# Kernel tuning notes

Hardware: AMD Instinct MI355X
Metric: run time of the kernel (lower is better)

Reference implementation:

```python
import jax, jax.numpy as jnp
import numpy as np

N = 50000
E = 800000
IN_C, HID_C, OUT_C = 128, 256, 2


def sage_conv(x, src, dst, W_l, b_l, W_r, num_nodes):
    # PyG SAGEConv with mean aggregation:
    #   out = lin_l(mean_{j in N(i)} x_j) + lin_r(x_i)
    msg = x[src]                                            # [E, d] gather
    agg = jax.ops.segment_sum(msg, dst, num_segments=num_nodes)   # [N, d]
    cnt = jax.ops.segment_sum(jnp.ones((msg.shape[0],), x.dtype), dst,
                              num_segments=num_nodes)        # [N]
    agg = agg / jnp.maximum(cnt, 1.0)[:, None]               # mean (deg>=1)
    return agg @ W_l.T + b_l + x @ W_r.T


def setup_inputs() -> dict:
    key = jax.random.key(0)
    ks = jax.random.split(key, 8)
    x = jax.random.normal(ks[0], (N, IN_C), dtype=jnp.float32)
    edge_index = jax.random.randint(ks[1], (2, E), 0, N, dtype=jnp.int32)
    # glorot-ish scaled params
    s1 = 1.0 / np.sqrt(IN_C)
    s2 = 1.0 / np.sqrt(HID_C)
    W1l = jax.random.normal(ks[2], (HID_C, IN_C), dtype=jnp.float32) * s1
    W1r = jax.random.normal(ks[3], (HID_C, IN_C), dtype=jnp.float32) * s1
    b1 = jnp.zeros((HID_C,), dtype=jnp.float32)
    W2l = jax.random.normal(ks[4], (OUT_C, HID_C), dtype=jnp.float32) * s2
    W2r = jax.random.normal(ks[5], (OUT_C, HID_C), dtype=jnp.float32) * s2
    b2 = jnp.zeros((OUT_C,), dtype=jnp.float32)
    return {"x": x, "edge_index": edge_index,
            "W1l": W1l, "b1": b1, "W1r": W1r,
            "W2l": W2l, "b2": b2, "W2r": W2r}


def reference(x, edge_index, W1l, b1, W1r, W2l, b2, W2r):
    src, dst = edge_index[0], edge_index[1]
    h = sage_conv(x, src, dst, W1l, b1, W1r, N)
    h = jax.nn.relu(h)
    out = sage_conv(h, src, dst, W2l, b2, W2r, N)
    return out
```

## Files before the change

kernel.cpp:

```cpp
#include <hip/hip_runtime.h>
#include <hip/hip_bf16.h>


#define IN_C 128
#define HID_C 256
#define BKT_SHIFT 7
#define BKT_W 128
#define CAP 3072

typedef __attribute__((ext_vector_type(8))) short short8;
typedef __attribute__((ext_vector_type(4))) float f32x4;

static __device__ __forceinline__ unsigned short f2b(float f) {
    __hip_bfloat16 h = __float2bfloat16(f);
    return *(unsigned short*)&h;
}
static __device__ __forceinline__ float b2f(unsigned short u) {
    unsigned v = ((unsigned)u) << 16;
    return *(float*)&v;
}

__global__ __launch_bounds__(512) void scatter_conv(
    const float* __restrict__ x, unsigned int* __restrict__ Abf,
    const float* __restrict__ w1l, const float* __restrict__ w1r,
    unsigned short* __restrict__ Bg,
    const int* __restrict__ ei, int* __restrict__ bcnt,
    unsigned int* __restrict__ binned,
    int npairs , int xblk, int E_) {
    __shared__ int hist[512];
    __shared__ int lbase[512];
    const int tid = threadIdx.x;
    if (blockIdx.x < xblk) {
        int t = blockIdx.x * 512 + tid;
        if (t >= npairs) return;
        float2 v = *(const float2*)&x[(size_t)t * 2];
        unsigned int o = ((unsigned)f2b(v.y) << 16) | f2b(v.x);
        int node = t >> 6, g = t & 63;
        Abf[(size_t)node * 128 + 64 + g] = o;
    } else if (blockIdx.x < xblk + 128) {
        int idx = (blockIdx.x - xblk) * 512 + tid;
        int o = idx >> 8, k = idx & 255;
        float f = (k < IN_C) ? w1l[o * IN_C + k] : w1r[o * IN_C + (k - IN_C)];
        Bg[idx] = f2b(f);
    } else {
        const int e0 = (blockIdx.x - xblk - 128) * 2048;
        hist[tid] = 0;
        __syncthreads();
        int dreg[4];
#pragma unroll
        for (int j = 0; j < 4; ++j) {
            int e = e0 + j * 512 + tid;
            dreg[j] = (e < E_) ? ei[E_ + e] : -1;
            if (dreg[j] >= 0) atomicAdd(&hist[dreg[j] >> BKT_SHIFT], 1);
        }
        __syncthreads();
        {
            int c = hist[tid];
            lbase[tid] = c ? tid * CAP + atomicAdd(&bcnt[tid], c) : 0;
            hist[tid] = 0;
        }
        __syncthreads();
#pragma unroll
        for (int j = 0; j < 4; ++j) {
            int e = e0 + j * 512 + tid;
            if (dreg[j] >= 0) {
                int d = dreg[j];
                int b = d >> BKT_SHIFT;
                int pos = lbase[b] + atomicAdd(&hist[b], 1);
                if (pos < b * CAP + CAP)
                    binned[pos] = ((unsigned)ei[e] << BKT_SHIFT) |
                                  (unsigned)(d & (BKT_W - 1));
            }
        }
    }
}


__global__ __launch_bounds__(1024) void sort_gather(
    unsigned int* __restrict__ binned, const int* __restrict__ bcnt,
    const uint4* __restrict__ abf4c, uint4* __restrict__ Abf4,
    int* __restrict__ deg, int* __restrict__ boffs, int n) {
    __shared__ unsigned int ebuf[CAP];
    __shared__ unsigned short sbuf[CAP];
    __shared__ int hist[BKT_W];
    __shared__ int offs[BKT_W];
    __shared__ int cur[BKT_W];
    const int tid = threadIdx.x;
    const int lane = tid & 63;
    const int bkt = blockIdx.x;
    const int gbase = bkt * CAP;
    int cnt = bcnt[bkt];
    if (cnt > CAP) cnt = CAP;

    if (tid < BKT_W) hist[tid] = 0;
    for (int i = tid; i < cnt; i += 1024) ebuf[i] = binned[gbase + i];
    __syncthreads();
    for (int i = tid; i < cnt; i += 1024)
        atomicAdd(&hist[ebuf[i] & (BKT_W - 1)], 1);
    __syncthreads();
    if (tid < 64) {
        int h0 = hist[lane * 2], h1 = hist[lane * 2 + 1];
        int s = h0 + h1;
        int incl = s;
#pragma unroll
        for (int off = 1; off < 64; off <<= 1) {
            int t = __shfl_up(incl, off);
            if (lane >= off) incl += t;
        }
        int excl = incl - s;
        offs[lane * 2] = excl;          cur[lane * 2] = excl;
        offs[lane * 2 + 1] = excl + h0; cur[lane * 2 + 1] = excl + h0;
    }
    __syncthreads();
    for (int i = tid; i < cnt; i += 1024) {
        unsigned int pk = ebuf[i];
        int pos = atomicAdd(&cur[pk & (BKT_W - 1)], 1);
        sbuf[pos] = (unsigned short)(pk >> BKT_SHIFT);
    }
    if (tid < BKT_W) {
        int node = bkt * BKT_W + tid;
        if (node < n) { deg[node] = hist[tid]; boffs[node] = offs[tid]; }
    }
    __syncthreads();

    {
        unsigned short* sout = (unsigned short*)(binned + gbase);
        for (int i = tid; i < cnt; i += 1024) sout[i] = sbuf[i];
    }

    const int wv = tid >> 6;
    const int ep = lane >> 4;
    const int pos = lane & 15;
    for (int ld = wv * 8; ld < wv * 8 + 8; ++ld) {
        int node = bkt * BKT_W + ld;
        if (node >= n) break;
        int beg = offs[ld], end = offs[ld] + hist[ld];
        float s[8] = {0.f, 0.f, 0.f, 0.f, 0.f, 0.f, 0.f, 0.f};
        for (int e = beg; e < end; e += 8) {
#pragma unroll
            for (int g = 0; g < 2; ++g) {
                int eg = e + g * 4 + ep;
                if (eg < end) {
                    int src = sbuf[eg];
                    uint4 u = abf4c[(size_t)src * 32 + 16 + pos];
                    s[0] += b2f(u.x & 0xffff); s[1] += b2f(u.x >> 16);
                    s[2] += b2f(u.y & 0xffff); s[3] += b2f(u.y >> 16);
                    s[4] += b2f(u.z & 0xffff); s[5] += b2f(u.z >> 16);
                    s[6] += b2f(u.w & 0xffff); s[7] += b2f(u.w >> 16);
                }
            }
        }
#pragma unroll
        for (int i = 0; i < 8; ++i) {
            s[i] += __shfl_xor(s[i], 16);
            s[i] += __shfl_xor(s[i], 32);
        }
        if (ep == 0) {
            float inv = 1.0f / (float)max(end - beg, 1);
            uint4 o;
            o.x = ((unsigned)f2b(s[1] * inv) << 16) | f2b(s[0] * inv);
            o.y = ((unsigned)f2b(s[3] * inv) << 16) | f2b(s[2] * inv);
            o.z = ((unsigned)f2b(s[5] * inv) << 16) | f2b(s[4] * inv);
            o.w = ((unsigned)f2b(s[7] * inv) << 16) | f2b(s[6] * inv);
            Abf4[(size_t)node * 32 + pos] = o;
        }
    }
}


#define LSTR 72

__global__ __launch_bounds__(256) void gemm1_fused(
    const unsigned short* __restrict__ Abf, const unsigned short* __restrict__ Bg,
    const float* __restrict__ b1, const float* __restrict__ w2l,
    const float* __restrict__ w2r, float* __restrict__ p2g,
    float* __restrict__ rsg, int nn) {
    __shared__ short As[128 * LSTR];
    __shared__ short Bs[128 * LSTR];

    const int tid = threadIdx.x;
    const int lane = tid & 63;
    const int wid = tid >> 6;
    const int wm = wid >> 1, wn = wid & 1;
    const int row0 = blockIdx.x * 128;
    const int col0 = blockIdx.y * 128;

    const int srow = tid >> 1;
    const int skc = (tid & 1) * 32;
    int arow = row0 + srow;
    if (arow >= nn) arow = nn - 1;
    const size_t agoff = (size_t)arow * 256 + skc;
    const size_t bgoff = (size_t)(col0 + srow) * 256 + skc;

    f32x4 acc[4][4];
#pragma unroll
    for (int i = 0; i < 4; ++i)
#pragma unroll
        for (int j = 0; j < 4; ++j) acc[i][j] = (f32x4){0.f, 0.f, 0.f, 0.f};

    const int quad = lane >> 4;
    const int l16 = lane & 15;

    for (int k0 = 0; k0 < 256; k0 += 64) {
        const uint4* ga = (const uint4*)(Abf + agoff + k0);
        const uint4* gb = (const uint4*)(Bg + bgoff + k0);
        uint4 va0 = ga[0], va1 = ga[1], va2 = ga[2], va3 = ga[3];
        uint4 vb0 = gb[0], vb1 = gb[1], vb2 = gb[2], vb3 = gb[3];

        __syncthreads();
        uint4* la = (uint4*)&As[srow * LSTR + skc];
        uint4* lb = (uint4*)&Bs[srow * LSTR + skc];
        la[0] = va0; la[1] = va1; la[2] = va2; la[3] = va3;
        lb[0] = vb0; lb[1] = vb1; lb[2] = vb2; lb[3] = vb3;
        __syncthreads();

#pragma unroll
        for (int kb = 0; kb < 2; ++kb) {
            short8 af[4], bf[4];
#pragma unroll
            for (int mt = 0; mt < 4; ++mt)
                af[mt] = *(const short8*)&As[(wm * 64 + mt * 16 + l16) * LSTR + kb * 32 + quad * 8];
#pragma unroll
            for (int nt = 0; nt < 4; ++nt)
                bf[nt] = *(const short8*)&Bs[(wn * 64 + nt * 16 + l16) * LSTR + kb * 32 + quad * 8];
#pragma unroll
            for (int mt = 0; mt < 4; ++mt)
#pragma unroll
                for (int nt = 0; nt < 4; ++nt)
                    acc[mt][nt] = __builtin_amdgcn_mfma_f32_16x16x32_bf16(
                        af[mt], bf[nt], acc[mt][nt], 0, 0, 0);
        }
    }

    const int cbase = col0 + wn * 64 + l16;
#pragma unroll
    for (int half = 0; half < 2; ++half) {
        const float* wA = half ? w2r : w2l;
        float* og = half ? rsg : p2g;
        f32x4 part[2][4];
#pragma unroll
        for (int c = 0; c < 2; ++c)
#pragma unroll
            for (int mt = 0; mt < 4; ++mt) part[c][mt] = (f32x4){0.f, 0.f, 0.f, 0.f};
#pragma unroll
        for (int nt = 0; nt < 4; ++nt) {
            const int col = cbase + nt * 16;
            const float bias = b1[col];
            const float w0 = wA[col];
            const float w1 = wA[HID_C + col];
#pragma unroll
            for (int mt = 0; mt < 4; ++mt)
#pragma unroll
                for (int r = 0; r < 4; ++r) {
                    float hv = fmaxf(acc[mt][nt][r] + bias, 0.0f);
                    part[0][mt][r] += hv * w0;
                    part[1][mt][r] += hv * w1;
                }
        }
#pragma unroll
        for (int c = 0; c < 2; ++c)
#pragma unroll
            for (int mt = 0; mt < 4; ++mt)
#pragma unroll
                for (int r = 0; r < 4; ++r)
#pragma unroll
                    for (int m = 1; m < 16; m <<= 1)
                        part[c][mt][r] += __shfl_xor(part[c][mt][r], m);
        if (l16 < 8) {
            const int ch2 = l16 & 1;
            const int mts = l16 >> 1;
#pragma unroll
            for (int r = 0; r < 4; ++r) {
                int row = row0 + wm * 64 + quad * 4 + mts * 16 + r;
                if (row < nn)
                    atomicAdd(&og[row * 2 + ch2], part[ch2][mts][r]);
            }
        }
    }
}


__global__ __launch_bounds__(256) void fin_bucket(
    const unsigned int* __restrict__ binned, const int* __restrict__ boffs,
    const int* __restrict__ deg,
    const float2* __restrict__ p2, const float2* __restrict__ rs,
    const float* __restrict__ b2, float* __restrict__ out, int n) {
    __shared__ float ps0[BKT_W];
    __shared__ float ps1[BKT_W];
    const int tid = threadIdx.x;
    const int ln = tid & (BKT_W - 1);
    const int hp = tid >> 7;
    const int bkt = blockIdx.x;
    const int node = bkt * BKT_W + ln;
    const unsigned short* sp =
        (const unsigned short*)(binned + (size_t)bkt * CAP);
    float s0 = 0.f, s1 = 0.f;
    int dg = 0;
    if (node < n) {
        int beg = boffs[node];
        dg = deg[node];
        int end = beg + dg;
        for (int i = beg + hp; i < end; i += 2) {
            float2 v = p2[sp[i]];
            s0 += v.x; s1 += v.y;
        }
    }
    if (hp) { ps0[ln] = s0; ps1[ln] = s1; }
    __syncthreads();
    if (!hp && node < n) {
        s0 += ps0[ln]; s1 += ps1[ln];
        float inv = 1.0f / (float)max(dg, 1);
        float2 self = rs[node];
        out[node * 2 + 0] = s0 * inv + self.x + b2[0];
        out[node * 2 + 1] = s1 * inv + self.y + b2[1];
    }
}


extern "C" void kernel_launch(void* const* d_in, const int* in_sizes, int n_in,
                              void* d_out, int out_size, void* d_ws, size_t ws_size,
                              hipStream_t stream) {
    const float* x   = (const float*)d_in[0];
    const int*   ei  = (const int*)d_in[1];
    const float* W1l = (const float*)d_in[2];
    const float* b1  = (const float*)d_in[3];
    const float* W1r = (const float*)d_in[4];
    const float* W2l = (const float*)d_in[5];
    const float* b2  = (const float*)d_in[6];
    const float* W2r = (const float*)d_in[7];
    float* out = (float*)d_out;

    const int N_ = in_sizes[0] / IN_C;
    const int E_ = in_sizes[1] / 2;
    const int nbkt = (N_ + BKT_W - 1) / BKT_W;

    char* wsb = (char*)d_ws;
    size_t off = 0;
    auto alloc = [&](size_t bytes) {
        void* ptr = wsb + off;
        off += ((bytes + 15) & ~(size_t)15);
        return ptr;
    };
    unsigned short* Abf = (unsigned short*)alloc((size_t)N_ * 256 * 2);
    unsigned short* Bg  = (unsigned short*)alloc(256 * 256 * 2);
    unsigned int* binned = (unsigned int*)alloc((size_t)(nbkt + 1) * CAP * 4);
    int*   bcnt = (int*)alloc(512 * 4);
    float* p2f  = (float*)alloc((size_t)N_ * 2 * 4);
    float* rsf  = (float*)alloc((size_t)N_ * 2 * 4);
    int*   deg  = (int*)alloc((size_t)N_ * 4);
    int*   boffs = (int*)alloc((size_t)N_ * 4);

    const int xblk = (N_ * 64 + 511) / 512;
    const int eblk = (E_ + 2047) / 2048;

    hipMemsetAsync(bcnt, 0, 512 * sizeof(int) + (size_t)N_ * 2 * 4 * 2, stream);

    scatter_conv<<<xblk + 128 + eblk, 512, 0, stream>>>(
        x, (unsigned int*)Abf, W1l, W1r, Bg, ei, bcnt, binned,
        N_ * 64, xblk, E_);

    sort_gather<<<nbkt, 1024, 0, stream>>>(binned, bcnt, (const uint4*)Abf,
                                           (uint4*)Abf, deg, boffs, N_);

    gemm1_fused<<<dim3((N_ + 127) / 128, 2), 256, 0, stream>>>(
        Abf, Bg, b1, W2l, W2r, p2f, rsf, N_);

    fin_bucket<<<nbkt, 256, 0, stream>>>(binned, boffs, deg,
                                         (const float2*)p2f, (const float2*)rsf,
                                         b2, out, N_);
}
```

Before: 185.3 us.

## Compute full hidden width per GEMM block, reduce epilogue in LDS, widen gather loops

The GEMM now uses 512-thread blocks that cover all 256 hidden columns for a 128-row tile. A block no longer splits the columns with a neighbour, so the layer-2 projections are reduced in shared memory with LDS atomics and written once, not with global atomics. That also removes the memset of the p2/rs buffers. The sort_gather inner loop is unrolled to 16 edges per iteration, and fin_bucket uses 4 threads per node instead of 2. The trade-off is more LDS per block and fewer GEMM blocks, which may lower occupancy.

```diff
diff --git a/kernel.cpp b/kernel.cpp
--- a/kernel.cpp
+++ b/kernel.cpp
@@ -136,9 +136,9 @@
         if (node >= n) break;
         int beg = offs[ld], end = offs[ld] + hist[ld];
         float s[8] = {0.f, 0.f, 0.f, 0.f, 0.f, 0.f, 0.f, 0.f};
-        for (int e = beg; e < end; e += 8) {
-#pragma unroll
-            for (int g = 0; g < 2; ++g) {
+        for (int e = beg; e < end; e += 16) {
+#pragma unroll
+            for (int g = 0; g < 4; ++g) {
                 int eg = e + g * 4 + ep;
                 if (eg < end) {
                     int src = sbuf[eg];
@@ -170,27 +170,26 @@
 
 #define LSTR 72
 
-__global__ __launch_bounds__(256) void gemm1_fused(
+__global__ __launch_bounds__(512) void gemm1_fused(
     const unsigned short* __restrict__ Abf, const unsigned short* __restrict__ Bg,
     const float* __restrict__ b1, const float* __restrict__ w2l,
-    const float* __restrict__ w2r, float* __restrict__ p2g,
-    float* __restrict__ rsg, int nn) {
+    const float* __restrict__ w2r, float2* __restrict__ p2g,
+    float2* __restrict__ rsg, int nn) {
     __shared__ short As[128 * LSTR];
-    __shared__ short Bs[128 * LSTR];
+    __shared__ short Bs[256 * LSTR];
 
     const int tid = threadIdx.x;
     const int lane = tid & 63;
     const int wid = tid >> 6;
-    const int wm = wid >> 1, wn = wid & 1;
+    const int wm = wid >> 2, wn = wid & 3;
     const int row0 = blockIdx.x * 128;
-    const int col0 = blockIdx.y * 128;
-
-    const int srow = tid >> 1;
-    const int skc = (tid & 1) * 32;
-    int arow = row0 + srow;
+
+    const int a_row = tid >> 2, a_seg = tid & 3;
+    int arow = row0 + a_row;
     if (arow >= nn) arow = nn - 1;
-    const size_t agoff = (size_t)arow * 256 + skc;
-    const size_t bgoff = (size_t)(col0 + srow) * 256 + skc;
+    const size_t agoff = (size_t)arow * 256 + a_seg * 16;
+    const int b_row = tid >> 1, b_seg = tid & 1;
+    const size_t bgoff = (size_t)b_row * 256 + b_seg * 32;
 
     f32x4 acc[4][4];
 #pragma unroll
@@ -204,13 +203,13 @@
     for (int k0 = 0; k0 < 256; k0 += 64) {
         const uint4* ga = (const uint4*)(Abf + agoff + k0);
         const uint4* gb = (const uint4*)(Bg + bgoff + k0);
-        uint4 va0 = ga[0], va1 = ga[1], va2 = ga[2], va3 = ga[3];
+        uint4 va0 = ga[0], va1 = ga[1];
         uint4 vb0 = gb[0], vb1 = gb[1], vb2 = gb[2], vb3 = gb[3];
 
         __syncthreads();
-        uint4* la = (uint4*)&As[srow * LSTR + skc];
-        uint4* lb = (uint4*)&Bs[srow * LSTR + skc];
-        la[0] = va0; la[1] = va1; la[2] = va2; la[3] = va3;
+        uint4* la = (uint4*)&As[a_row * LSTR + a_seg * 16];
+        la[0] = va0; la[1] = va1;
+        uint4* lb = (uint4*)&Bs[b_row * LSTR + b_seg * 32];
         lb[0] = vb0; lb[1] = vb1; lb[2] = vb2; lb[3] = vb3;
         __syncthreads();
 
@@ -232,11 +231,15 @@
         }
     }
 
-    const int cbase = col0 + wn * 64 + l16;
+    float* pr = (float*)As;
+    __syncthreads();
+    pr[tid % 512] = 0.f;
+    __syncthreads();
+
+    const int cbase = wn * 64 + l16;
 #pragma unroll
     for (int half = 0; half < 2; ++half) {
         const float* wA = half ? w2r : w2l;
-        float* og = half ? rsg : p2g;
         f32x4 part[2][4];
 #pragma unroll
         for (int c = 0; c < 2; ++c)
@@ -271,22 +274,31 @@
             const int mts = l16 >> 1;
 #pragma unroll
             for (int r = 0; r < 4; ++r) {
-                int row = row0 + wm * 64 + quad * 4 + mts * 16 + r;
-                if (row < nn)
-                    atomicAdd(&og[row * 2 + ch2], part[ch2][mts][r]);
+                int rloc = wm * 64 + quad * 4 + mts * 16 + r;
+                atomicAdd(&pr[rloc * 4 + half * 2 + ch2], part[ch2][mts][r]);
             }
         }
     }
-}
-
-
-__global__ __launch_bounds__(256) void fin_bucket(
+    __syncthreads();
+    if (tid < 256) {
+        int rloc = tid >> 1, pair = tid & 1;
+        int row = row0 + rloc;
+        if (row < nn) {
+            float2 v = make_float2(pr[rloc * 4 + pair * 2],
+                                   pr[rloc * 4 + pair * 2 + 1]);
+            if (pair) rsg[row] = v; else p2g[row] = v;
+        }
+    }
+}
+
+
+__global__ __launch_bounds__(512) void fin_bucket(
     const unsigned int* __restrict__ binned, const int* __restrict__ boffs,
     const int* __restrict__ deg,
     const float2* __restrict__ p2, const float2* __restrict__ rs,
     const float* __restrict__ b2, float* __restrict__ out, int n) {
-    __shared__ float ps0[BKT_W];
-    __shared__ float ps1[BKT_W];
+    __shared__ float ps0[3][BKT_W];
+    __shared__ float ps1[3][BKT_W];
     const int tid = threadIdx.x;
     const int ln = tid & (BKT_W - 1);
     const int hp = tid >> 7;
@@ -300,15 +312,16 @@
         int beg = boffs[node];
         dg = deg[node];
         int end = beg + dg;
-        for (int i = beg + hp; i < end; i += 2) {
+        for (int i = beg + hp; i < end; i += 4) {
             float2 v = p2[sp[i]];
             s0 += v.x; s1 += v.y;
         }
     }
-    if (hp) { ps0[ln] = s0; ps1[ln] = s1; }
+    if (hp) { ps0[hp - 1][ln] = s0; ps1[hp - 1][ln] = s1; }
     __syncthreads();
     if (!hp && node < n) {
-        s0 += ps0[ln]; s1 += ps1[ln];
+        s0 += ps0[0][ln] + ps0[1][ln] + ps0[2][ln];
+        s1 += ps1[0][ln] + ps1[1][ln] + ps1[2][ln];
         float inv = 1.0f / (float)max(dg, 1);
         float2 self = rs[node];
         out[node * 2 + 0] = s0 * inv + self.x + b2[0];
@@ -353,7 +366,7 @@
     const int xblk = (N_ * 64 + 511) / 512;
     const int eblk = (E_ + 2047) / 2048;
 
-    hipMemsetAsync(bcnt, 0, 512 * sizeof(int) + (size_t)N_ * 2 * 4 * 2, stream);
+    hipMemsetAsync(bcnt, 0, 512 * sizeof(int), stream);
 
     scatter_conv<<<xblk + 128 + eblk, 512, 0, stream>>>(
         x, (unsigned int*)Abf, W1l, W1r, Bg, ei, bcnt, binned,
@@ -362,10 +375,10 @@
     sort_gather<<<nbkt, 1024, 0, stream>>>(binned, bcnt, (const uint4*)Abf,
                                            (uint4*)Abf, deg, boffs, N_);
 
-    gemm1_fused<<<dim3((N_ + 127) / 128, 2), 256, 0, stream>>>(
-        Abf, Bg, b1, W2l, W2r, p2f, rsf, N_);
-
-    fin_bucket<<<nbkt, 256, 0, stream>>>(binned, boffs, deg,
+    gemm1_fused<<<(N_ + 127) / 128, 512, 0, stream>>>(
+        Abf, Bg, b1, W2l, W2r, (float2*)p2f, (float2*)rsf, N_);
+
+    fin_bucket<<<nbkt, 512, 0, stream>>>(binned, boffs, deg,
                                          (const float2*)p2f, (const float2*)rsf,
                                          b2, out, N_);
 }
```

After: 179.1 us. 3.3% less time.
